# Kernel tuning notes

Measured on AMD Instinct MI355X. Metric: run time of the kernel, lower is better.

The kernel has to match this reference:

```python
import jax, jax.numpy as jnp
import numpy as np

N_NODES = 10000
N_EDGES = 160000
F_IN = 2613
D = 256
H = 4
NEG_SLOPE = 0.2
BN_EPS = 1e-5


def _bn(h, g, b):
    # BatchNorm1d in training mode: batch statistics, biased variance
    return (h - h.mean(0)) / jnp.sqrt(h.var(0) + BN_EPS) * g + b


def _gat_conv(h_in, src, dst, n, W, att_src, att_dst, bias):
    # PyG GATConv, concat=True: h_in [n, F] -> [n, H*D]
    h = (h_in @ W).reshape(n, H, D)                      # [n, H, D]
    a_src = jnp.sum(h * att_src, axis=-1)                # [n, H]
    a_dst = jnp.sum(h * att_dst, axis=-1)                # [n, H]
    e = jax.nn.leaky_relu(a_src[src] + a_dst[dst], NEG_SLOPE)  # [E, H]
    # segment softmax over destination nodes (stable)
    m = jax.ops.segment_max(e, dst, num_segments=n)
    e = jnp.exp(e - m[dst])
    denom = jax.ops.segment_sum(e, dst, num_segments=n)
    alpha = e / (denom[dst] + 1e-16)                     # [E, H]
    out = jax.ops.segment_sum(h[src] * alpha[:, :, None], dst, num_segments=n)
    return out.reshape(n, H * D) + bias


def setup_inputs() -> dict:
    key = jax.random.key(0)
    ks = jax.random.split(key, 24)
    s = 0.02
    inp = {
        "x": jax.random.normal(ks[0], (N_NODES, F_IN), jnp.float32),
        "edges": jax.random.randint(ks[1], (2, N_EDGES), 0, N_NODES, jnp.int64),
        # MLP stack
        "W1": jax.random.normal(ks[2], (F_IN, D), jnp.float32) * s,
        "b1": jnp.zeros((D,), jnp.float32),
        "W2": jax.random.normal(ks[3], (D, D), jnp.float32) * s,
        "b2": jnp.zeros((D,), jnp.float32),
        "W3": jax.random.normal(ks[4], (D, D), jnp.float32) * s,
        "b3": jnp.zeros((D,), jnp.float32),
        # BatchNorm affine params
        "g1": jnp.ones((D,), jnp.float32), "be1": jnp.zeros((D,), jnp.float32),
        "g2": jnp.ones((D,), jnp.float32), "be2": jnp.zeros((D,), jnp.float32),
        "g3": jnp.ones((D,), jnp.float32), "be3": jnp.zeros((D,), jnp.float32),
        "g4": jnp.ones((H * D,), jnp.float32), "be4": jnp.zeros((H * D,), jnp.float32),
        "Wg1": jax.random.normal(ks[5], (D, H * D), jnp.float32) * s,
        "as1": jax.random.normal(ks[6], (H, D), jnp.float32) * s,
        "ad1": jax.random.normal(ks[7], (H, D), jnp.float32) * s,
        "bg1": jnp.zeros((H * D,), jnp.float32),
        "Wg2": jax.random.normal(ks[8], (H * D, H * D), jnp.float32) * s,
        "as2": jax.random.normal(ks[9], (H, D), jnp.float32) * s,
        "ad2": jax.random.normal(ks[10], (H, D), jnp.float32) * s,
        "bg2": jnp.zeros((H * D,), jnp.float32),
    }
    return inp


def reference(x, edges, W1, b1, W2, b2, W3, b3,
              g1, be1, g2, be2, g3, be3, g4, be4,
              Wg1, as1, ad1, bg1, Wg2, as2, ad2, bg2):
    n = x.shape[0]
    src, dst = edges[0], edges[1]
    # PyG: remove existing self-loops then add one per node. We reroute
    # accidental self-loops deterministically, then append self-loops.
    dst = jnp.where(src == dst, (dst + 1) % n, dst)
    loops = jnp.arange(n, dtype=src.dtype)
    src = jnp.concatenate([src, loops])
    dst = jnp.concatenate([dst, loops])

    h = jax.nn.elu(_bn(x @ W1 + b1, g1, be1))
    h = jax.nn.elu(_bn(h @ W2 + b2, g2, be2))
    h = jax.nn.elu(_bn(h @ W3 + b3, g3, be3))
    h = _gat_conv(h, src, dst, n, Wg1, as1, ad1, bg1)
    h = jax.nn.elu(_bn(h, g4, be4))
    h = _gat_conv(h, src, dst, n, Wg2, as2, ad2, bg2)
    return h
```

## Files before the change

kernel.cpp:

```cpp
#include <hip/hip_runtime.h>
#include <hip/hip_bf16.h>

typedef __attribute__((ext_vector_type(8))) short short8v;
typedef __attribute__((ext_vector_type(4))) float f32x4;

__device__ inline float b2f(ushort u) {
  union { uint i; float f; } c;
  c.i = (uint)u << 16;
  return c.f;
}
__device__ inline ushort f2b(float f) {
  __hip_bfloat16 h = __float2bfloat16(f);
  return *(ushort*)&h;
}

template <bool BN, bool ALIGNED, bool SPLIT, bool B16O>
__global__ __launch_bounds__(256) void gemm_bn(
    const float* __restrict__ A, const __hip_bfloat16* __restrict__ Bh,
    const __hip_bfloat16* __restrict__ Bl, const float* __restrict__ sc,
    const float* __restrict__ sh, float* __restrict__ P,
    ushort* __restrict__ Pb, int M, int N, int K, int Kp, int nc, int nr,
    int nz) {
  constexpr int NARR = SPLIT ? 4 : 2;
  __shared__ ushort lds[NARR][128][40];
  ushort(*Ash)[40] = lds[0];
  ushort(*Bsh)[40] = lds[1];
  ushort(*Asl)[40] = lds[SPLIT ? 2 : 0];
  ushort(*Bsl)[40] = lds[SPLIT ? 3 : 0];
  const int nwg = gridDim.x;
  const int b = blockIdx.x;
  const int l = (b & 7) * (nwg >> 3) + (b >> 3);
  const int cb = l % nc;
  const int rr = (l / nc) % nr;
  const int z = l / (nc * nr);

  const int tid = threadIdx.x;
  const int lane = tid & 63;
  const int w = tid >> 6, wr = w >> 1, wc = w & 1;
  const int brow = rr * 128, bcol = cb * 128;
  const int l15 = lane & 15, koff = (lane >> 4) * 8;
  const int arow = tid >> 1, aseg = (tid & 1) * 16;
  const int nK = (K + 31) >> 5;
  const int ks0 = (nK * z) / nz, ks1 = (nK * (z + 1)) / nz;

  f32x4 acc[4][4] = {};

  const int ar = brow + arow;
  const bool arv = ar < M;
  const float* Arow = A + (long)ar * K;
  const __hip_bfloat16* BrowH = Bh + (long)(bcol + arow) * Kp;
  const __hip_bfloat16* BrowL = SPLIT ? Bl + (long)(bcol + arow) * Kp : nullptr;

  for (int ks = ks0; ks < ks1; ++ks) {
    const int k0 = ks << 5;
    const int kbase = k0 + aseg;
    float av[16];
    if (arv) {
      if (ALIGNED) {
        const float4* ap = (const float4*)(Arow + kbase);
#pragma unroll
        for (int q = 0; q < 4; ++q) {
          float4 f = ap[q];
          av[q * 4 + 0] = f.x;
          av[q * 4 + 1] = f.y;
          av[q * 4 + 2] = f.z;
          av[q * 4 + 3] = f.w;
        }
      } else {
        if (kbase + 16 <= K) {
#pragma unroll
          for (int j = 0; j < 16; ++j) av[j] = Arow[kbase + j];
        } else {
#pragma unroll
          for (int j = 0; j < 16; ++j)
            av[j] = (kbase + j < K) ? Arow[kbase + j] : 0.f;
        }
      }
      if (BN) {
#pragma unroll
        for (int q = 0; q < 4; ++q) {
          float4 c4 = *(const float4*)(sc + kbase + q * 4);
          float4 h4 = *(const float4*)(sh + kbase + q * 4);
          float* a4 = &av[q * 4];
          a4[0] = fmaf(a4[0], c4.x, h4.x);
          a4[1] = fmaf(a4[1], c4.y, h4.y);
          a4[2] = fmaf(a4[2], c4.z, h4.z);
          a4[3] = fmaf(a4[3], c4.w, h4.w);
        }
#pragma unroll
        for (int j = 0; j < 16; ++j) {
          float v = av[j];
          av[j] = v > 0.f ? v : (__expf(v) - 1.f);
        }
      }
    } else {
#pragma unroll
      for (int j = 0; j < 16; ++j) av[j] = 0.f;
    }
    short8v ah0, ah1, al0, al1;
    if (SPLIT) {
#pragma unroll
      for (int j = 0; j < 8; ++j) {
        {
          uint u = __float_as_uint(av[j]);
          ah0[j] = (short)(u >> 16);
          al0[j] = (short)f2b(av[j] - __uint_as_float(u & 0xFFFF0000u));
        }
        {
          uint u = __float_as_uint(av[j + 8]);
          ah1[j] = (short)(u >> 16);
          al1[j] = (short)f2b(av[j + 8] - __uint_as_float(u & 0xFFFF0000u));
        }
      }
    } else {
#pragma unroll
      for (int j = 0; j < 8; ++j) {
        ah0[j] = (short)f2b(av[j]);
        ah1[j] = (short)f2b(av[j + 8]);
      }
    }
    short8v bh0 = *(const short8v*)(BrowH + kbase);
    short8v bh1 = *(const short8v*)(BrowH + kbase + 8);
    short8v bl0, bl1;
    if (SPLIT) {
      bl0 = *(const short8v*)(BrowL + kbase);
      bl1 = *(const short8v*)(BrowL + kbase + 8);
    }
    __syncthreads();
    *(short8v*)&Ash[arow][aseg] = ah0;
    *(short8v*)&Ash[arow][aseg + 8] = ah1;
    *(short8v*)&Bsh[arow][aseg] = bh0;
    *(short8v*)&Bsh[arow][aseg + 8] = bh1;
    if (SPLIT) {
      *(short8v*)&Asl[arow][aseg] = al0;
      *(short8v*)&Asl[arow][aseg + 8] = al1;
      *(short8v*)&Bsl[arow][aseg] = bl0;
      *(short8v*)&Bsl[arow][aseg + 8] = bl1;
    }
    __syncthreads();

    short8v bfh[4], bfl[4];
#pragma unroll
    for (int nn = 0; nn < 4; ++nn) {
      bfh[nn] = *(const short8v*)&Bsh[wc * 64 + nn * 16 + l15][koff];
      if (SPLIT) bfl[nn] = *(const short8v*)&Bsl[wc * 64 + nn * 16 + l15][koff];
    }
#pragma unroll
    for (int m = 0; m < 4; ++m) {
      short8v afh = *(const short8v*)&Ash[wr * 64 + m * 16 + l15][koff];
      short8v afl;
      if (SPLIT) afl = *(const short8v*)&Asl[wr * 64 + m * 16 + l15][koff];
#pragma unroll
      for (int nn = 0; nn < 4; ++nn) {
        acc[m][nn] = __builtin_amdgcn_mfma_f32_16x16x32_bf16(afh, bfh[nn], acc[m][nn], 0, 0, 0);
        if (SPLIT) {
          acc[m][nn] = __builtin_amdgcn_mfma_f32_16x16x32_bf16(afh, bfl[nn], acc[m][nn], 0, 0, 0);
          acc[m][nn] = __builtin_amdgcn_mfma_f32_16x16x32_bf16(afl, bfh[nn], acc[m][nn], 0, 0, 0);
        }
      }
    }
  }

  float* outp = P + (long)z * M * N;
#pragma unroll
  for (int m = 0; m < 4; ++m) {
#pragma unroll
    for (int nn = 0; nn < 4; ++nn) {
      int col = bcol + wc * 64 + nn * 16 + l15;
#pragma unroll
      for (int r = 0; r < 4; ++r) {
        int row = brow + wr * 64 + m * 16 + (lane >> 4) * 4 + r;
        if (row < M) {
          if (B16O)
            Pb[(long)row * N + col] = f2b(acc[m][nn][r]);
          else
            outp[(long)row * N + col] = acc[m][nn][r];
        }
      }
    }
  }
}

template <bool BIAS, bool STATS>
__global__ __launch_bounds__(256) void reduce_post(
    const float* __restrict__ P, const float* __restrict__ bias,
    float* __restrict__ C, float* __restrict__ osum, float* __restrict__ osq,
    long MN, int N, int Z) {
  const int col = (int)((blockIdx.x * 256 + threadIdx.x) % N);
  const float bv = BIAS ? bias[col] : 0.f;
  float ps = 0.f, pq = 0.f;
  for (long i = blockIdx.x * 256LL + threadIdx.x; i < MN;
       i += (long)gridDim.x * 256LL) {
    float s = bv;
    for (int zz = 0; zz < Z; ++zz) s += P[(long)zz * MN + i];
    C[i] = s;
    if (STATS) {
      ps += s;
      pq += s * s;
    }
  }
  if (STATS) {
    atomicAdd(&osum[col], ps);
    atomicAdd(&osq[col], pq);
  }
}

__global__ __launch_bounds__(256) void bn_coef(
    const float* __restrict__ ssum, const float* __restrict__ ssq,
    const float* __restrict__ g, const float* __restrict__ be,
    float* __restrict__ sc, float* __restrict__ sh, int N, float invM) {
  int c = blockIdx.x * 256 + threadIdx.x;
  if (c >= N) return;
  float mean = ssum[c] * invM;
  float var = ssq[c] * invM - mean * mean;
  float s = rsqrtf(var + 1e-5f) * g[c];
  sc[c] = s;
  sh[c] = be[c] - mean * s;
}

template <bool LO>
__global__ __launch_bounds__(256) void trans_split(
    const float* __restrict__ W, __hip_bfloat16* __restrict__ Oh,
    __hip_bfloat16* __restrict__ Ol, int K, int N, int Kp) {
  __shared__ float tile[64][65];
  const int k0 = blockIdx.x * 64, n0 = blockIdx.y * 64;
  const int tx = threadIdx.x & 63, ty = threadIdx.x >> 6;
#pragma unroll
  for (int j = 0; j < 16; ++j) {
    int r = ty * 16 + j;
    int k = k0 + r;
    tile[r][tx] = (k < K) ? W[(long)k * N + n0 + tx] : 0.f;
  }
  __syncthreads();
#pragma unroll
  for (int j = 0; j < 16; ++j) {
    int a = ty * 16 + j;
    float v = tile[tx][a];
    long o = (long)(n0 + a) * Kp + k0 + tx;
    if (LO) {
      uint u = __float_as_uint(v);
      ushort hu = (ushort)(u >> 16);
      Oh[o] = *(__hip_bfloat16*)&hu;
      ushort lu = f2b(v - __uint_as_float(u & 0xFFFF0000u));
      Ol[o] = *(__hip_bfloat16*)&lu;
    } else {
      ushort hu = f2b(v);
      Oh[o] = *(__hip_bfloat16*)&hu;
    }
  }
}

__global__ __launch_bounds__(256) void bn_stats(
    const float* __restrict__ h, int M, int N, float* __restrict__ sum,
    float* __restrict__ sumsq) {
  int col = blockIdx.y * 256 + threadIdx.x;
  float s = 0.f, sq = 0.f;
  for (int r = blockIdx.x; r < M; r += gridDim.x) {
    float v = h[(long)r * N + col];
    s += v;
    sq += v * v;
  }
  atomicAdd(&sum[col], s);
  atomicAdd(&sumsq[col], sq);
}

__global__ __launch_bounds__(256) void att_scores_bf16(
    const ushort* __restrict__ hgb, const float* __restrict__ att_s,
    const float* __restrict__ att_d, float* __restrict__ a_src,
    float* __restrict__ a_dst, int n) {
  int node = blockIdx.x;
  int h = threadIdx.x >> 6, lane = threadIdx.x & 63;
  int c = lane * 4;
  ushort4 hv = *(const ushort4*)(hgb + (long)node * 1024 + h * 256 + c);
  float4 as = *(const float4*)(att_s + h * 256 + c);
  float4 ad = *(const float4*)(att_d + h * 256 + c);
  float x0 = b2f(hv.x), x1 = b2f(hv.y), x2 = b2f(hv.z), x3 = b2f(hv.w);
  float ss = x0 * as.x + x1 * as.y + x2 * as.z + x3 * as.w;
  float sd = x0 * ad.x + x1 * ad.y + x2 * ad.z + x3 * ad.w;
#pragma unroll
  for (int off = 32; off; off >>= 1) {
    ss += __shfl_down(ss, off);
    sd += __shfl_down(sd, off);
  }
  if (lane == 0) {
    a_src[node * 4 + h] = ss;
    a_dst[node * 4 + h] = sd;
  }
}

__global__ __launch_bounds__(256) void deg_count(
    const int* __restrict__ srcA, const int* __restrict__ dstA,
    int* __restrict__ deg, int n, int E0, int E) {
  int e = blockIdx.x * blockDim.x + threadIdx.x;
  if (e >= E) return;
  int d;
  if (e < E0) {
    int s = srcA[e];
    d = dstA[e];
    if (s == d) d = (d + 1) % n;
  } else {
    d = e - E0;
  }
  atomicAdd(&deg[d], 1);
}

__global__ __launch_bounds__(256) void scan_rows(
    const int* __restrict__ deg, int* __restrict__ row_start, int n) {
  __shared__ int sums[256];
  int t = threadIdx.x;
  int chunk = (n + 255) / 256;
  int start = t * chunk, end = min(start + chunk, n);
  int s = 0;
  for (int i = start; i < end; ++i) s += deg[i];
  sums[t] = s;
  __syncthreads();
  for (int off = 1; off < 256; off <<= 1) {
    int v = (t >= off) ? sums[t - off] : 0;
    __syncthreads();
    sums[t] += v;
    __syncthreads();
  }
  int run = (t == 0) ? 0 : sums[t - 1];
  for (int i = start; i < end; ++i) {
    row_start[i] = run;
    run += deg[i];
  }
  if (t == 255) row_start[n] = run;
}

__global__ __launch_bounds__(256) void scatter_edges(
    const int* __restrict__ srcA, const int* __restrict__ dstA,
    int* __restrict__ cursor, int* __restrict__ csr_src, int n, int E0, int E) {
  int e = blockIdx.x * blockDim.x + threadIdx.x;
  if (e >= E) return;
  int s, d;
  if (e < E0) {
    s = srcA[e];
    d = dstA[e];
    if (s == d) d = (d + 1) % n;
  } else {
    s = d = e - E0;
  }
  int pos = atomicAdd(&cursor[d], 1);
  csr_src[pos] = s;
}

__global__ __launch_bounds__(256) void aggregate_fused(
    const ushort* __restrict__ hgb, const int* __restrict__ row_start,
    const int* __restrict__ csr_src, const float* __restrict__ a_src,
    const float* __restrict__ a_dst, const float* __restrict__ bias,
    float* __restrict__ out) {
  int d = blockIdx.x;
  int t = threadIdx.x;
  int hh = t >> 6;
  int off = hh * 256 + (t & 63) * 4;
  int p0 = row_start[d], p1 = row_start[d + 1];
  float adv = a_dst[d * 4 + hh];
  float den = 1e-16f;
  float4 acc = {0.f, 0.f, 0.f, 0.f};
  for (int p = p0; p < p1; ++p) {
    int s = csr_src[p];
    float v = a_src[s * 4 + hh] + adv;
    v = v > 0.f ? v : 0.2f * v;
    float ex = __expf(v);
    den += ex;
    ushort4 hv = *(const ushort4*)(hgb + (long)s * 1024 + off);
    acc.x += ex * b2f(hv.x);
    acc.y += ex * b2f(hv.y);
    acc.z += ex * b2f(hv.z);
    acc.w += ex * b2f(hv.w);
  }
  float rden = 1.f / den;
  float4 bv = *(const float4*)(bias + off);
  float4 o;
  o.x = bv.x + acc.x * rden;
  o.y = bv.y + acc.y * rden;
  o.z = bv.z + acc.z * rden;
  o.w = bv.w + acc.w * rden;
  *(float4*)(out + (long)d * 1024 + off) = o;
}

extern "C" void kernel_launch(void* const* d_in, const int* in_sizes, int n_in,
                              void* d_out, int out_size, void* d_ws,
                              size_t ws_size, hipStream_t stream) {
  const float* x = (const float*)d_in[0];
  const int* edges = (const int*)d_in[1];
  const float* W1 = (const float*)d_in[2];
  const float* b1 = (const float*)d_in[3];
  const float* W2 = (const float*)d_in[4];
  const float* b2 = (const float*)d_in[5];
  const float* W3 = (const float*)d_in[6];
  const float* b3 = (const float*)d_in[7];
  const float* g1 = (const float*)d_in[8];
  const float* be1 = (const float*)d_in[9];
  const float* g2 = (const float*)d_in[10];
  const float* be2 = (const float*)d_in[11];
  const float* g3 = (const float*)d_in[12];
  const float* be3 = (const float*)d_in[13];
  const float* g4 = (const float*)d_in[14];
  const float* be4 = (const float*)d_in[15];
  const float* Wg1 = (const float*)d_in[16];
  const float* as1 = (const float*)d_in[17];
  const float* ad1 = (const float*)d_in[18];
  const float* bg1 = (const float*)d_in[19];
  const float* Wg2 = (const float*)d_in[20];
  const float* as2 = (const float*)d_in[21];
  const float* ad2 = (const float*)d_in[22];
  const float* bg2 = (const float*)d_in[23];
  float* out = (float*)d_out;

  const int n = 10000, E0 = 160000, E = 170000;
  const int F = 2613, Fp = 2624, D = 256, HD = 1024;
  const int* srcA = edges;
  const int* dstA = edges + E0;

  uint8_t* p = (uint8_t*)d_ws;
  auto alloc = [&](size_t bytes) -> void* {
    void* r = (void*)p;
    p += (bytes + 255) & ~(size_t)255;
    return r;
  };
  float* h1 = (float*)alloc((size_t)n * D * 4);
  float* h2 = (float*)alloc((size_t)n * D * 4);
  float* h3 = (float*)alloc((size_t)n * D * 4);
  float* agg = (float*)alloc((size_t)n * HD * 4);
  float* pbuf = (float*)alloc((size_t)4 * n * D * 4);
  ushort* hgb = (ushort*)alloc((size_t)n * HD * 2);
  __hip_bfloat16* W1h = (__hip_bfloat16*)alloc((size_t)D * Fp * 2);
  __hip_bfloat16* W1l = (__hip_bfloat16*)alloc((size_t)D * Fp * 2);
  __hip_bfloat16* W2h = (__hip_bfloat16*)alloc((size_t)D * D * 2);
  __hip_bfloat16* W2l = (__hip_bfloat16*)alloc((size_t)D * D * 2);
  __hip_bfloat16* W3h = (__hip_bfloat16*)alloc((size_t)D * D * 2);
  __hip_bfloat16* W3l = (__hip_bfloat16*)alloc((size_t)D * D * 2);
  __hip_bfloat16* Wg1h = (__hip_bfloat16*)alloc((size_t)HD * D * 2);
  __hip_bfloat16* Wg2h = (__hip_bfloat16*)alloc((size_t)HD * HD * 2);
  float* asrc = (float*)alloc((size_t)n * 4 * 4);
  float* adst = (float*)alloc((size_t)n * 4 * 4);
  float* sc1 = (float*)alloc(D * 4);
  float* sh1 = (float*)alloc(D * 4);
  float* sc2 = (float*)alloc(D * 4);
  float* sh2 = (float*)alloc(D * 4);
  float* sc3 = (float*)alloc(D * 4);
  float* sh3 = (float*)alloc(D * 4);
  float* sc4 = (float*)alloc(HD * 4);
  float* sh4 = (float*)alloc(HD * 4);
  int* row_start = (int*)alloc((size_t)(n + 1) * 4);
  int* cursor = (int*)alloc((size_t)n * 4);
  int* csr_src = (int*)alloc((size_t)E * 4);
  uint8_t* z0 = p;
  float* ssum1 = (float*)alloc(D * 4);
  float* ssq1 = (float*)alloc(D * 4);
  float* ssum2 = (float*)alloc(D * 4);
  float* ssq2 = (float*)alloc(D * 4);
  float* ssum3 = (float*)alloc(D * 4);
  float* ssq3 = (float*)alloc(D * 4);
  float* ssum4 = (float*)alloc(HD * 4);
  float* ssq4 = (float*)alloc(HD * 4);
  int* deg = (int*)alloc((size_t)n * 4);
  size_t zbytes = (size_t)(p - z0);

  dim3 blk(256);
  const int rb = (n + 127) / 128;
  const int eb = (E + 255) / 256;
  const long MN_D = (long)n * D;
  const float invM = 1.f / (float)n;
  const int gMLP = 2 * rb * 4;
  const int gGAT = 8 * rb * 1;

  hipMemsetAsync(z0, 0, zbytes, stream);

  deg_count<<<eb, blk, 0, stream>>>(srcA, dstA, deg, n, E0, E);
  scan_rows<<<1, blk, 0, stream>>>(deg, row_start, n);
  hipMemcpyAsync(cursor, row_start, n * sizeof(int), hipMemcpyDeviceToDevice, stream);
  scatter_edges<<<eb, blk, 0, stream>>>(srcA, dstA, cursor, csr_src, n, E0, E);

  trans_split<true><<<dim3(Fp / 64, D / 64), blk, 0, stream>>>(W1, W1h, W1l, F, D, Fp);
  trans_split<true><<<dim3(D / 64, D / 64), blk, 0, stream>>>(W2, W2h, W2l, D, D, D);
  trans_split<true><<<dim3(D / 64, D / 64), blk, 0, stream>>>(W3, W3h, W3l, D, D, D);
  trans_split<false><<<dim3(D / 64, HD / 64), blk, 0, stream>>>(Wg1, Wg1h, nullptr, D, HD, D);
  trans_split<false><<<dim3(HD / 64, HD / 64), blk, 0, stream>>>(Wg2, Wg2h, nullptr, HD, HD, HD);

  gemm_bn<false, false, true, false><<<gMLP, blk, 0, stream>>>(
      x, W1h, W1l, nullptr, nullptr, pbuf, nullptr, n, D, F, Fp, 2, rb, 4);
  reduce_post<true, true><<<512, blk, 0, stream>>>(pbuf, b1, h1, ssum1, ssq1, MN_D, D, 4);
  bn_coef<<<1, blk, 0, stream>>>(ssum1, ssq1, g1, be1, sc1, sh1, D, invM);

  gemm_bn<true, true, true, false><<<gMLP, blk, 0, stream>>>(
      h1, W2h, W2l, sc1, sh1, pbuf, nullptr, n, D, D, D, 2, rb, 4);
  reduce_post<true, true><<<512, blk, 0, stream>>>(pbuf, b2, h2, ssum2, ssq2, MN_D, D, 4);
  bn_coef<<<1, blk, 0, stream>>>(ssum2, ssq2, g2, be2, sc2, sh2, D, invM);

  gemm_bn<true, true, true, false><<<gMLP, blk, 0, stream>>>(
      h2, W3h, W3l, sc2, sh2, pbuf, nullptr, n, D, D, D, 2, rb, 4);
  reduce_post<true, true><<<512, blk, 0, stream>>>(pbuf, b3, h3, ssum3, ssq3, MN_D, D, 4);
  bn_coef<<<1, blk, 0, stream>>>(ssum3, ssq3, g3, be3, sc3, sh3, D, invM);

  gemm_bn<true, true, false, true><<<gGAT, blk, 0, stream>>>(
      h3, Wg1h, nullptr, sc3, sh3, nullptr, hgb, n, HD, D, D, 8, rb, 1);
  att_scores_bf16<<<n, blk, 0, stream>>>(hgb, as1, ad1, asrc, adst, n);
  aggregate_fused<<<n, blk, 0, stream>>>(hgb, row_start, csr_src, asrc, adst, bg1, agg);

  bn_stats<<<dim3(64, HD / 256), blk, 0, stream>>>(agg, n, HD, ssum4, ssq4);
  bn_coef<<<4, blk, 0, stream>>>(ssum4, ssq4, g4, be4, sc4, sh4, HD, invM);

  gemm_bn<true, true, false, true><<<gGAT, blk, 0, stream>>>(
      agg, Wg2h, nullptr, sc4, sh4, nullptr, hgb, n, HD, HD, HD, 8, rb, 1);
  att_scores_bf16<<<n, blk, 0, stream>>>(hgb, as2, ad2, asrc, adst, n);
  aggregate_fused<<<n, blk, 0, stream>>>(hgb, row_start, csr_src, asrc, adst, bg2, out);
}
```

Baseline: 597.7 us.

## Unfuse BN+ELU into bf16 pre-pass for GAT GEMMs and double layer-1 split-K

```diff
diff --git a/kernel.cpp b/kernel.cpp
--- a/kernel.cpp
+++ b/kernel.cpp
@@ -14,19 +14,16 @@
   return *(ushort*)&h;
 }
 
-template <bool BN, bool ALIGNED, bool SPLIT, bool B16O>
+template <bool BN, bool ALIGNED>
 __global__ __launch_bounds__(256) void gemm_bn(
     const float* __restrict__ A, const __hip_bfloat16* __restrict__ Bh,
     const __hip_bfloat16* __restrict__ Bl, const float* __restrict__ sc,
-    const float* __restrict__ sh, float* __restrict__ P,
-    ushort* __restrict__ Pb, int M, int N, int K, int Kp, int nc, int nr,
-    int nz) {
-  constexpr int NARR = SPLIT ? 4 : 2;
-  __shared__ ushort lds[NARR][128][40];
-  ushort(*Ash)[40] = lds[0];
-  ushort(*Bsh)[40] = lds[1];
-  ushort(*Asl)[40] = lds[SPLIT ? 2 : 0];
-  ushort(*Bsl)[40] = lds[SPLIT ? 3 : 0];
+    const float* __restrict__ sh, float* __restrict__ P, int M, int N, int K,
+    int Kp, int nc, int nr, int nz) {
+  __shared__ ushort Ash[128][40];
+  __shared__ ushort Bsh[128][40];
+  __shared__ ushort Asl[128][40];
+  __shared__ ushort Bsl[128][40];
   const int nwg = gridDim.x;
   const int b = blockIdx.x;
   const int l = (b & 7) * (nwg >> 3) + (b >> 3);
@@ -49,7 +46,7 @@
   const bool arv = ar < M;
   const float* Arow = A + (long)ar * K;
   const __hip_bfloat16* BrowH = Bh + (long)(bcol + arow) * Kp;
-  const __hip_bfloat16* BrowL = SPLIT ? Bl + (long)(bcol + arow) * Kp : nullptr;
+  const __hip_bfloat16* BrowL = Bl + (long)(bcol + arow) * Kp;
 
   for (int ks = ks0; ks < ks1; ++ks) {
     const int k0 = ks << 5;
@@ -98,65 +95,49 @@
       for (int j = 0; j < 16; ++j) av[j] = 0.f;
     }
     short8v ah0, ah1, al0, al1;
-    if (SPLIT) {
-#pragma unroll
-      for (int j = 0; j < 8; ++j) {
-        {
-          uint u = __float_as_uint(av[j]);
-          ah0[j] = (short)(u >> 16);
-          al0[j] = (short)f2b(av[j] - __uint_as_float(u & 0xFFFF0000u));
-        }
-        {
-          uint u = __float_as_uint(av[j + 8]);
-          ah1[j] = (short)(u >> 16);
-          al1[j] = (short)f2b(av[j + 8] - __uint_as_float(u & 0xFFFF0000u));
-        }
-      }
-    } else {
-#pragma unroll
-      for (int j = 0; j < 8; ++j) {
-        ah0[j] = (short)f2b(av[j]);
-        ah1[j] = (short)f2b(av[j + 8]);
+#pragma unroll
+    for (int j = 0; j < 8; ++j) {
+      {
+        uint u = __float_as_uint(av[j]);
+        ah0[j] = (short)(u >> 16);
+        al0[j] = (short)f2b(av[j] - __uint_as_float(u & 0xFFFF0000u));
+      }
+      {
+        uint u = __float_as_uint(av[j + 8]);
+        ah1[j] = (short)(u >> 16);
+        al1[j] = (short)f2b(av[j + 8] - __uint_as_float(u & 0xFFFF0000u));
       }
     }
     short8v bh0 = *(const short8v*)(BrowH + kbase);
     short8v bh1 = *(const short8v*)(BrowH + kbase + 8);
-    short8v bl0, bl1;
-    if (SPLIT) {
-      bl0 = *(const short8v*)(BrowL + kbase);
-      bl1 = *(const short8v*)(BrowL + kbase + 8);
-    }
+    short8v bl0 = *(const short8v*)(BrowL + kbase);
+    short8v bl1 = *(const short8v*)(BrowL + kbase + 8);
     __syncthreads();
     *(short8v*)&Ash[arow][aseg] = ah0;
     *(short8v*)&Ash[arow][aseg + 8] = ah1;
     *(short8v*)&Bsh[arow][aseg] = bh0;
     *(short8v*)&Bsh[arow][aseg + 8] = bh1;
-    if (SPLIT) {
-      *(short8v*)&Asl[arow][aseg] = al0;
-      *(short8v*)&Asl[arow][aseg + 8] = al1;
-      *(short8v*)&Bsl[arow][aseg] = bl0;
-      *(short8v*)&Bsl[arow][aseg + 8] = bl1;
-    }
+    *(short8v*)&Asl[arow][aseg] = al0;
+    *(short8v*)&Asl[arow][aseg + 8] = al1;
+    *(short8v*)&Bsl[arow][aseg] = bl0;
+    *(short8v*)&Bsl[arow][aseg + 8] = bl1;
     __syncthreads();
 
     short8v bfh[4], bfl[4];
 #pragma unroll
     for (int nn = 0; nn < 4; ++nn) {
       bfh[nn] = *(const short8v*)&Bsh[wc * 64 + nn * 16 + l15][koff];
-      if (SPLIT) bfl[nn] = *(const short8v*)&Bsl[wc * 64 + nn * 16 + l15][koff];
+      bfl[nn] = *(const short8v*)&Bsl[wc * 64 + nn * 16 + l15][koff];
     }
 #pragma unroll
     for (int m = 0; m < 4; ++m) {
       short8v afh = *(const short8v*)&Ash[wr * 64 + m * 16 + l15][koff];
-      short8v afl;
-      if (SPLIT) afl = *(const short8v*)&Asl[wr * 64 + m * 16 + l15][koff];
+      short8v afl = *(const short8v*)&Asl[wr * 64 + m * 16 + l15][koff];
 #pragma unroll
       for (int nn = 0; nn < 4; ++nn) {
         acc[m][nn] = __builtin_amdgcn_mfma_f32_16x16x32_bf16(afh, bfh[nn], acc[m][nn], 0, 0, 0);
-        if (SPLIT) {
-          acc[m][nn] = __builtin_amdgcn_mfma_f32_16x16x32_bf16(afh, bfl[nn], acc[m][nn], 0, 0, 0);
-          acc[m][nn] = __builtin_amdgcn_mfma_f32_16x16x32_bf16(afl, bfh[nn], acc[m][nn], 0, 0, 0);
-        }
+        acc[m][nn] = __builtin_amdgcn_mfma_f32_16x16x32_bf16(afh, bfl[nn], acc[m][nn], 0, 0, 0);
+        acc[m][nn] = __builtin_amdgcn_mfma_f32_16x16x32_bf16(afl, bfh[nn], acc[m][nn], 0, 0, 0);
       }
     }
   }
@@ -170,14 +151,104 @@
 #pragma unroll
       for (int r = 0; r < 4; ++r) {
         int row = brow + wr * 64 + m * 16 + (lane >> 4) * 4 + r;
-        if (row < M) {
-          if (B16O)
-            Pb[(long)row * N + col] = f2b(acc[m][nn][r]);
-          else
-            outp[(long)row * N + col] = acc[m][nn][r];
-        }
-      }
-    }
+        if (row < M) outp[(long)row * N + col] = acc[m][nn][r];
+      }
+    }
+  }
+}
+
+__global__ __launch_bounds__(256) void gemm_bf16(
+    const ushort* __restrict__ A, const __hip_bfloat16* __restrict__ B,
+    ushort* __restrict__ C, int M, int N, int K, int nc, int nr) {
+  __shared__ ushort Ash[128][40];
+  __shared__ ushort Bsh[128][40];
+  const int nwg = gridDim.x;
+  const int b = blockIdx.x;
+  const int l = (b & 7) * (nwg >> 3) + (b >> 3);
+  const int cb = l % nc;
+  const int rr = l / nc;
+
+  const int tid = threadIdx.x;
+  const int lane = tid & 63;
+  const int w = tid >> 6, wr = w >> 1, wc = w & 1;
+  const int brow = rr * 128, bcol = cb * 128;
+  const int l15 = lane & 15, koff = (lane >> 4) * 8;
+  const int arow = tid >> 1, aseg = (tid & 1) * 16;
+  const int nK = K >> 5;
+
+  f32x4 acc[4][4] = {};
+  const short8v zz = {};
+
+  const int ar = brow + arow;
+  const bool arv = ar < M;
+  const ushort* Arow = A + (long)ar * K;
+  const ushort* Brow = (const ushort*)B + (long)(bcol + arow) * K;
+
+  for (int ks = 0; ks < nK; ++ks) {
+    const int kbase = (ks << 5) + aseg;
+    short8v a0 = arv ? *(const short8v*)(Arow + kbase) : zz;
+    short8v a1 = arv ? *(const short8v*)(Arow + kbase + 8) : zz;
+    short8v b0 = *(const short8v*)(Brow + kbase);
+    short8v b1 = *(const short8v*)(Brow + kbase + 8);
+    __syncthreads();
+    *(short8v*)&Ash[arow][aseg] = a0;
+    *(short8v*)&Ash[arow][aseg + 8] = a1;
+    *(short8v*)&Bsh[arow][aseg] = b0;
+    *(short8v*)&Bsh[arow][aseg + 8] = b1;
+    __syncthreads();
+
+    short8v bf[4];
+#pragma unroll
+    for (int nn = 0; nn < 4; ++nn)
+      bf[nn] = *(const short8v*)&Bsh[wc * 64 + nn * 16 + l15][koff];
+#pragma unroll
+    for (int m = 0; m < 4; ++m) {
+      short8v af = *(const short8v*)&Ash[wr * 64 + m * 16 + l15][koff];
+#pragma unroll
+      for (int nn = 0; nn < 4; ++nn)
+        acc[m][nn] = __builtin_amdgcn_mfma_f32_16x16x32_bf16(af, bf[nn], acc[m][nn], 0, 0, 0);
+    }
+  }
+
+#pragma unroll
+  for (int m = 0; m < 4; ++m) {
+#pragma unroll
+    for (int nn = 0; nn < 4; ++nn) {
+      int col = bcol + wc * 64 + nn * 16 + l15;
+#pragma unroll
+      for (int r = 0; r < 4; ++r) {
+        int row = brow + wr * 64 + m * 16 + (lane >> 4) * 4 + r;
+        if (row < M) C[(long)row * N + col] = f2b(acc[m][nn][r]);
+      }
+    }
+  }
+}
+
+__global__ __launch_bounds__(256) void bn_elu_b16(
+    const float* __restrict__ h, const float* __restrict__ sc,
+    const float* __restrict__ sh, ushort* __restrict__ o, long MN, int N) {
+  long nq = MN >> 2;
+  for (long q = blockIdx.x * 256LL + threadIdx.x; q < nq;
+       q += (long)gridDim.x * 256LL) {
+    long i = q << 2;
+    int col = (int)(i % N);
+    float4 v = *(const float4*)(h + i);
+    float4 c = *(const float4*)(sc + col);
+    float4 s = *(const float4*)(sh + col);
+    float a0 = fmaf(v.x, c.x, s.x);
+    float a1 = fmaf(v.y, c.y, s.y);
+    float a2 = fmaf(v.z, c.z, s.z);
+    float a3 = fmaf(v.w, c.w, s.w);
+    a0 = a0 > 0.f ? a0 : (__expf(a0) - 1.f);
+    a1 = a1 > 0.f ? a1 : (__expf(a1) - 1.f);
+    a2 = a2 > 0.f ? a2 : (__expf(a2) - 1.f);
+    a3 = a3 > 0.f ? a3 : (__expf(a3) - 1.f);
+    ushort4 r;
+    r.x = f2b(a0);
+    r.y = f2b(a1);
+    r.z = f2b(a2);
+    r.w = f2b(a3);
+    *(ushort4*)(o + i) = r;
   }
 }
 
@@ -424,8 +495,9 @@
   float* h2 = (float*)alloc((size_t)n * D * 4);
   float* h3 = (float*)alloc((size_t)n * D * 4);
   float* agg = (float*)alloc((size_t)n * HD * 4);
-  float* pbuf = (float*)alloc((size_t)4 * n * D * 4);
+  float* pbuf = (float*)alloc((size_t)8 * n * D * 4);
   ushort* hgb = (ushort*)alloc((size_t)n * HD * 2);
+  ushort* actb = (ushort*)alloc((size_t)n * HD * 2);
   __hip_bfloat16* W1h = (__hip_bfloat16*)alloc((size_t)D * Fp * 2);
   __hip_bfloat16* W1l = (__hip_bfloat16*)alloc((size_t)D * Fp * 2);
   __hip_bfloat16* W2h = (__hip_bfloat16*)alloc((size_t)D * D * 2);
@@ -463,9 +535,11 @@
   const int rb = (n + 127) / 128;
   const int eb = (E + 255) / 256;
   const long MN_D = (long)n * D;
+  const long MN_HD = (long)n * HD;
   const float invM = 1.f / (float)n;
+  const int gL1 = 2 * rb * 8;
   const int gMLP = 2 * rb * 4;
-  const int gGAT = 8 * rb * 1;
+  const int gGAT = 8 * rb;
 
   hipMemsetAsync(z0, 0, zbytes, stream);
 
@@ -480,31 +554,31 @@
   trans_split<false><<<dim3(D / 64, HD / 64), blk, 0, stream>>>(Wg1, Wg1h, nullptr, D, HD, D);
   trans_split<false><<<dim3(HD / 64, HD / 64), blk, 0, stream>>>(Wg2, Wg2h, nullptr, HD, HD, HD);
 
-  gemm_bn<false, false, true, false><<<gMLP, blk, 0, stream>>>(
-      x, W1h, W1l, nullptr, nullptr, pbuf, nullptr, n, D, F, Fp, 2, rb, 4);
-  reduce_post<true, true><<<512, blk, 0, stream>>>(pbuf, b1, h1, ssum1, ssq1, MN_D, D, 4);
+  gemm_bn<false, false><<<gL1, blk, 0, stream>>>(
+      x, W1h, W1l, nullptr, nullptr, pbuf, n, D, F, Fp, 2, rb, 8);
+  reduce_post<true, true><<<512, blk, 0, stream>>>(pbuf, b1, h1, ssum1, ssq1, MN_D, D, 8);
   bn_coef<<<1, blk, 0, stream>>>(ssum1, ssq1, g1, be1, sc1, sh1, D, invM);
 
-  gemm_bn<true, true, true, false><<<gMLP, blk, 0, stream>>>(
-      h1, W2h, W2l, sc1, sh1, pbuf, nullptr, n, D, D, D, 2, rb, 4);
+  gemm_bn<true, true><<<gMLP, blk, 0, stream>>>(
+      h1, W2h, W2l, sc1, sh1, pbuf, n, D, D, D, 2, rb, 4);
   reduce_post<true, true><<<512, blk, 0, stream>>>(pbuf, b2, h2, ssum2, ssq2, MN_D, D, 4);
   bn_coef<<<1, blk, 0, stream>>>(ssum2, ssq2, g2, be2, sc2, sh2, D, invM);
 
-  gemm_bn<true, true, true, false><<<gMLP, blk, 0, stream>>>(
-      h2, W3h, W3l, sc2, sh2, pbuf, nullptr, n, D, D, D, 2, rb, 4);
+  gemm_bn<true, true><<<gMLP, blk, 0, stream>>>(
+      h2, W3h, W3l, sc2, sh2, pbuf, n, D, D, D, 2, rb, 4);
   reduce_post<true, true><<<512, blk, 0, stream>>>(pbuf, b3, h3, ssum3, ssq3, MN_D, D, 4);
   bn_coef<<<1, blk, 0, stream>>>(ssum3, ssq3, g3, be3, sc3, sh3, D, invM);
 
-  gemm_bn<true, true, false, true><<<gGAT, blk, 0, stream>>>(
-      h3, Wg1h, nullptr, sc3, sh3, nullptr, hgb, n, HD, D, D, 8, rb, 1);
+  bn_elu_b16<<<1024, blk, 0, stream>>>(h3, sc3, sh3, actb, MN_D, D);
+  gemm_bf16<<<gGAT, blk, 0, stream>>>(actb, Wg1h, hgb, n, HD, D, 8, rb);
   att_scores_bf16<<<n, blk, 0, stream>>>(hgb, as1, ad1, asrc, adst, n);
   aggregate_fused<<<n, blk, 0, stream>>>(hgb, row_start, csr_src, asrc, adst, bg1, agg);
 
   bn_stats<<<dim3(64, HD / 256), blk, 0, stream>>>(agg, n, HD, ssum4, ssq4);
   bn_coef<<<4, blk, 0, stream>>>(ssum4, ssq4, g4, be4, sc4, sh4, HD, invM);
-
-  gemm_bn<true, true, false, true><<<gGAT, blk, 0, stream>>>(
-      agg, Wg2h, nullptr, sc4, sh4, nullptr, hgb, n, HD, HD, HD, 8, rb, 1);
+  bn_elu_b16<<<2048, blk, 0, stream>>>(agg, sc4, sh4, actb, MN_HD, HD);
+
+  gemm_bf16<<<gGAT, blk, 0, stream>>>(actb, Wg2h, hgb, n, HD, HD, 8, rb);
   att_scores_bf16<<<n, blk, 0, stream>>>(hgb, as2, ad2, asrc, adst, n);
   aggregate_fused<<<n, blk, 0, stream>>>(hgb, row_start, csr_src, asrc, adst, bg2, out);
 }
```

After: 572.7 us. 4.2% less time.
